# Kernel tuning notes

Hardware: AMD Instinct MI355X
Metric: run time of the kernel (lower is better)

The kernel has to match this reference:

```python
import jax, jax.numpy as jnp
import numpy as np

B, N = 128, 1024


def setup_inputs() -> dict:
    key = jax.random.key(0)
    k1, k2 = jax.random.split(key)
    vector = jax.random.uniform(k1, (B, N), dtype=jnp.float32)
    interactions = jax.random.normal(k2, (N, N), dtype=jnp.float32)
    return {"vector": vector, "interactions": interactions}


def reference(vector, interactions):
    # x: [B,1,N], y: [B,N,1] -> broadcast dirac delta [B,N,N]
    x = vector[:, None, :]
    y = vector[:, :, None]
    dd = (1.0 - x) * (1.0 - y) + x * y  # [B,N,N]
    dd = jnp.triu(dd)                   # keep upper triangle incl. diagonal
    energy = dd * interactions          # [B,N,N] * [N,N] broadcast
    return energy.reshape(vector.shape[0], -1).sum(axis=1)  # [B]
```

## Files before the change

### kernel.cpp

```cpp
#include <hip/hip_runtime.h>
#include <math.h>

#define NDIM 1024
#define BDIM 128
#define TS 32
#define NT (NDIM / TS)
#define NTILES (NT * (NT + 1) / 2)

__global__ __launch_bounds__(256) void potts_main(
    const float* __restrict__ V,
    const float* __restrict__ W,
    float* __restrict__ partial)
{
    const int t = blockIdx.x;
    const int u = NTILES - 1 - t;
    int kk = (int)(0.5f * (sqrtf((float)(8 * u + 1)) - 1.0f));
    if (kk * (kk + 1) / 2 > u) --kk;
    if ((kk + 1) * (kk + 2) / 2 <= u) ++kk;
    const int ti = NT - 1 - kk;
    const int tj = NT - 1 - (u - kk * (kk + 1) / 2);
    const int I0 = ti * TS, J0 = tj * TS;
    const bool diag = (ti == tj);

    __shared__ float4 vj4[BDIM][8];
    __shared__ float4 vi4[BDIM][8];
    __shared__ float rs[TS];
    __shared__ float red[4][BDIM];

    const int tid = threadIdx.x;
    const int w = tid >> 6;
    const int l = tid & 63;
    const int l7 = l & 7;

    {
        const int r = tid >> 3, c4 = (tid & 7) * 4;
        float4 w4 = *(const float4*)(W + (size_t)(I0 + r) * NDIM + (J0 + c4));
        if (diag) {
            if (c4 + 0 < r) w4.x = 0.0f;
            if (c4 + 1 < r) w4.y = 0.0f;
            if (c4 + 2 < r) w4.z = 0.0f;
            if (c4 + 3 < r) w4.w = 0.0f;
        }
        float rsum = (w4.x + w4.y) + (w4.z + w4.w);
        rsum += __shfl_xor(rsum, 1);
        rsum += __shfl_xor(rsum, 2);
        rsum += __shfl_xor(rsum, 4);
        if ((tid & 7) == 0) rs[r] = rsum;
    }

#pragma unroll
    for (int it = 0; it < 4; ++it) {
        const int fid = tid + 256 * it;
        const int b = fid >> 3, j4 = fid & 7;
        const int g = j4 ^ (b & 7);
        vj4[b][g] = *(const float4*)(V + (size_t)b * NDIM + (J0 + 4 * j4));
        vi4[b][g] = *(const float4*)(V + (size_t)b * NDIM + (I0 + 4 * j4));
    }
    __syncthreads();

    float vj0[TS], vj1[TS];
#pragma unroll
    for (int j4 = 0; j4 < 8; ++j4) {
        const int g = j4 ^ l7;
        const float4 a = vj4[l][g];
        vj0[4*j4+0] = a.x; vj0[4*j4+1] = a.y;
        vj0[4*j4+2] = a.z; vj0[4*j4+3] = a.w;
        const float4 c = vj4[l + 64][g];
        vj1[4*j4+0] = c.x; vj1[4*j4+1] = c.y;
        vj1[4*j4+2] = c.z; vj1[4*j4+3] = c.w;
    }
    float vi0[8], vi1[8];
    {
        const int ga = (2 * w) ^ l7, gb = (2 * w + 1) ^ l7;
        const float4 p  = vi4[l][ga],      q  = vi4[l][gb];
        const float4 p1 = vi4[l + 64][ga], q1 = vi4[l + 64][gb];
        vi0[0]=p.x;  vi0[1]=p.y;  vi0[2]=p.z;  vi0[3]=p.w;
        vi0[4]=q.x;  vi0[5]=q.y;  vi0[6]=q.z;  vi0[7]=q.w;
        vi1[0]=p1.x; vi1[1]=p1.y; vi1[2]=p1.z; vi1[3]=p1.w;
        vi1[4]=q1.x; vi1[5]=q1.y; vi1[6]=q1.z; vi1[7]=q1.w;
    }

    float acc0 = 0.0f, acc1 = 0.0f;
#pragma unroll
    for (int k = 0; k < 8; ++k) {
        const int i = 8 * w + k;
        const float* __restrict__ wrow = W + (size_t)(I0 + i) * NDIM + J0;
        float za0 = 0.f, zb0 = 0.f, za1 = 0.f, zb1 = 0.f;
#pragma unroll
        for (int j = 0; j < TS; j += 2) {
            float wa = wrow[j];
            float wb = wrow[j + 1];
            if (diag) {
                if (j < i)     wa = 0.0f;
                if (j + 1 < i) wb = 0.0f;
            }
            za0 = fmaf(wa, vj0[j],     za0);
            zb0 = fmaf(wb, vj0[j + 1], zb0);
            za1 = fmaf(wa, vj1[j],     za1);
            zb1 = fmaf(wb, vj1[j + 1], zb1);
        }
        const float y0 = vi0[k], y1 = vi1[k];
        const float rsk = rs[i];
        acc0 = fmaf(1.0f - y0, rsk, acc0);
        acc0 = fmaf(2.0f * y0 - 1.0f, za0 + zb0, acc0);
        acc1 = fmaf(1.0f - y1, rsk, acc1);
        acc1 = fmaf(2.0f * y1 - 1.0f, za1 + zb1, acc1);
    }

    red[w][l] = acc0;
    red[w][l + 64] = acc1;
    __syncthreads();
    if (tid < BDIM) {
        partial[t * BDIM + tid] =
            (red[0][tid] + red[1][tid]) + (red[2][tid] + red[3][tid]);
    }
}

__global__ __launch_bounds__(64) void potts_red(
    const float* __restrict__ partial, float* __restrict__ out)
{
    const int b = blockIdx.x;
    const int lane = threadIdx.x;
    float a0 = 0.f, a1 = 0.f;
    int t = lane;
#pragma unroll 4
    for (; t + 64 < NTILES; t += 128) {
        a0 += partial[t * BDIM + b];
        a1 += partial[(t + 64) * BDIM + b];
    }
    if (t < NTILES) a0 += partial[t * BDIM + b];
    float a = a0 + a1;
#pragma unroll
    for (int off = 32; off > 0; off >>= 1)
        a += __shfl_down(a, off);
    if (lane == 0) out[b] = a;
}

extern "C" void kernel_launch(void* const* d_in, const int* in_sizes, int n_in,
                              void* d_out, int out_size, void* d_ws, size_t ws_size,
                              hipStream_t stream) {
    const float* V = (const float*)d_in[0];
    const float* W = (const float*)d_in[1];
    float* out = (float*)d_out;
    float* partial = (float*)d_ws;

    potts_main<<<dim3(NTILES), dim3(256), 0, stream>>>(V, W, partial);
    potts_red<<<dim3(BDIM), dim3(64), 0, stream>>>(partial, out);
}
```

Baseline: 66.90 us.

## Fuse final reduction into main kernel via atomic slots and last-block finish

```diff
diff --git a/kernel.cpp b/kernel.cpp
--- a/kernel.cpp
+++ b/kernel.cpp
@@ -6,11 +6,14 @@
 #define TS 32
 #define NT (NDIM / TS)
 #define NTILES (NT * (NT + 1) / 2)
+#define NC 32
+#define CNT_OFF (NC * BDIM)
 
-__global__ __launch_bounds__(256) void potts_main(
+__global__ __launch_bounds__(256) void potts_fused(
     const float* __restrict__ V,
     const float* __restrict__ W,
-    float* __restrict__ partial)
+    float* __restrict__ ws,
+    float* __restrict__ out)
 {
     const int t = blockIdx.x;
     const int u = NTILES - 1 - t;
@@ -26,6 +29,7 @@
     __shared__ float4 vi4[BDIM][8];
     __shared__ float rs[TS];
     __shared__ float red[4][BDIM];
+    __shared__ int lastflag;
 
     const int tid = threadIdx.x;
     const int w = tid >> 6;
@@ -87,17 +91,35 @@
         const float* __restrict__ wrow = W + (size_t)(I0 + i) * NDIM + J0;
         float za0 = 0.f, zb0 = 0.f, za1 = 0.f, zb1 = 0.f;
 #pragma unroll
-        for (int j = 0; j < TS; j += 2) {
-            float wa = wrow[j];
-            float wb = wrow[j + 1];
+        for (int j4 = 0; j4 < 8; j4 += 2) {
+            float4 wa = *(const float4*)(wrow + 4 * j4);
+            float4 wb = *(const float4*)(wrow + 4 * j4 + 4);
             if (diag) {
-                if (j < i)     wa = 0.0f;
-                if (j + 1 < i) wb = 0.0f;
+                if (4*j4 + 0 < i) wa.x = 0.0f;
+                if (4*j4 + 1 < i) wa.y = 0.0f;
+                if (4*j4 + 2 < i) wa.z = 0.0f;
+                if (4*j4 + 3 < i) wa.w = 0.0f;
+                if (4*j4 + 4 < i) wb.x = 0.0f;
+                if (4*j4 + 5 < i) wb.y = 0.0f;
+                if (4*j4 + 6 < i) wb.z = 0.0f;
+                if (4*j4 + 7 < i) wb.w = 0.0f;
             }
-            za0 = fmaf(wa, vj0[j],     za0);
-            zb0 = fmaf(wb, vj0[j + 1], zb0);
-            za1 = fmaf(wa, vj1[j],     za1);
-            zb1 = fmaf(wb, vj1[j + 1], zb1);
+            za0 = fmaf(wa.x, vj0[4*j4+0], za0);
+            za0 = fmaf(wa.y, vj0[4*j4+1], za0);
+            za0 = fmaf(wa.z, vj0[4*j4+2], za0);
+            za0 = fmaf(wa.w, vj0[4*j4+3], za0);
+            za1 = fmaf(wa.x, vj1[4*j4+0], za1);
+            za1 = fmaf(wa.y, vj1[4*j4+1], za1);
+            za1 = fmaf(wa.z, vj1[4*j4+2], za1);
+            za1 = fmaf(wa.w, vj1[4*j4+3], za1);
+            zb0 = fmaf(wb.x, vj0[4*j4+4], zb0);
+            zb0 = fmaf(wb.y, vj0[4*j4+5], zb0);
+            zb0 = fmaf(wb.z, vj0[4*j4+6], zb0);
+            zb0 = fmaf(wb.w, vj0[4*j4+7], zb0);
+            zb1 = fmaf(wb.x, vj1[4*j4+4], zb1);
+            zb1 = fmaf(wb.y, vj1[4*j4+5], zb1);
+            zb1 = fmaf(wb.z, vj1[4*j4+6], zb1);
+            zb1 = fmaf(wb.w, vj1[4*j4+7], zb1);
         }
         const float y0 = vi0[k], y1 = vi1[k];
         const float rsk = rs[i];
@@ -110,30 +132,32 @@
     red[w][l] = acc0;
     red[w][l + 64] = acc1;
     __syncthreads();
+
+    float* slot = ws + (size_t)(t & (NC - 1)) * BDIM;
     if (tid < BDIM) {
-        partial[t * BDIM + tid] =
-            (red[0][tid] + red[1][tid]) + (red[2][tid] + red[3][tid]);
+        const float v4 = (red[0][tid] + red[1][tid]) + (red[2][tid] + red[3][tid]);
+        atomicAdd(slot + tid, v4);
     }
-}
 
-__global__ __launch_bounds__(64) void potts_red(
-    const float* __restrict__ partial, float* __restrict__ out)
-{
-    const int b = blockIdx.x;
-    const int lane = threadIdx.x;
-    float a0 = 0.f, a1 = 0.f;
-    int t = lane;
-#pragma unroll 4
-    for (; t + 64 < NTILES; t += 128) {
-        a0 += partial[t * BDIM + b];
-        a1 += partial[(t + 64) * BDIM + b];
+    __threadfence();
+    __syncthreads();
+    if (tid == 0) {
+        unsigned int* cnt = (unsigned int*)(ws + CNT_OFF);
+        const unsigned int old =
+            __hip_atomic_fetch_add(cnt, 1u, __ATOMIC_ACQ_REL,
+                                   __HIP_MEMORY_SCOPE_AGENT);
+        lastflag = (old == NTILES - 1) ? 1 : 0;
     }
-    if (t < NTILES) a0 += partial[t * BDIM + b];
-    float a = a0 + a1;
+    __syncthreads();
+    if (lastflag && tid < BDIM) {
+        float s = 0.0f;
 #pragma unroll
-    for (int off = 32; off > 0; off >>= 1)
-        a += __shfl_down(a, off);
-    if (lane == 0) out[b] = a;
+        for (int c = 0; c < NC; ++c) {
+            s += __hip_atomic_load(ws + (size_t)c * BDIM + tid,
+                                   __ATOMIC_RELAXED, __HIP_MEMORY_SCOPE_AGENT);
+        }
+        out[tid] = s;
+    }
 }
 
 extern "C" void kernel_launch(void* const* d_in, const int* in_sizes, int n_in,
@@ -142,8 +166,8 @@
     const float* V = (const float*)d_in[0];
     const float* W = (const float*)d_in[1];
     float* out = (float*)d_out;
-    float* partial = (float*)d_ws;
+    float* ws = (float*)d_ws;
 
-    potts_main<<<dim3(NTILES), dim3(256), 0, stream>>>(V, W, partial);
-    potts_red<<<dim3(BDIM), dim3(64), 0, stream>>>(partial, out);
+    hipMemsetAsync(d_ws, 0, (CNT_OFF + 16) * sizeof(float), stream);
+    potts_fused<<<dim3(NTILES), dim3(256), 0, stream>>>(V, W, ws, out);
 }
```

Measured after the change: 107.5 us. +60.7%, slower.
